# Performance work log

Measured on AMD Instinct MI355X. Metric: run time of the kernel, lower is better.

The kernel has to match this reference:

```python
import jax, jax.numpy as jnp
from jax import lax
import numpy as np

HIDDEN = 512
NUM_LAYERS = 2
NUM_KEYS = 128
BATCH = 256
SEQ = 512


def setup_inputs() -> dict:
    key = jax.random.key(0)
    ks = jax.random.split(key, 16)
    s = 0.05  # keep gates out of saturation
    inp = {
        "x": jax.random.normal(ks[0], (BATCH, SEQ, NUM_KEYS), dtype=jnp.float32),
        # layer 0 (input size NUM_KEYS); PyTorch gate order i,f,g,o stacked on dim0
        "W_ih0": jax.random.normal(ks[1], (4 * HIDDEN, NUM_KEYS), dtype=jnp.float32) * s,
        "W_hh0": jax.random.normal(ks[2], (4 * HIDDEN, HIDDEN), dtype=jnp.float32) * s,
        "b_ih0": jax.random.normal(ks[3], (4 * HIDDEN,), dtype=jnp.float32) * s,
        "b_hh0": jax.random.normal(ks[4], (4 * HIDDEN,), dtype=jnp.float32) * s,
        # layer 1 (input size HIDDEN)
        "W_ih1": jax.random.normal(ks[5], (4 * HIDDEN, HIDDEN), dtype=jnp.float32) * s,
        "W_hh1": jax.random.normal(ks[6], (4 * HIDDEN, HIDDEN), dtype=jnp.float32) * s,
        "b_ih1": jax.random.normal(ks[7], (4 * HIDDEN,), dtype=jnp.float32) * s,
        "b_hh1": jax.random.normal(ks[8], (4 * HIDDEN,), dtype=jnp.float32) * s,
        # final linear head
        "W_fc": jax.random.normal(ks[9], (NUM_KEYS, HIDDEN), dtype=jnp.float32) * s,
        "b_fc": jax.random.normal(ks[10], (NUM_KEYS,), dtype=jnp.float32) * s,
    }
    return inp


def _lstm_layer(xs, W_ih, W_hh, b_ih, b_hh):
    # xs: [B, T, in]. Precompute input contribution to all gates outside the scan.
    B = xs.shape[0]
    H = W_hh.shape[1]
    xg = jnp.einsum("bti,gi->btg", xs, W_ih) + b_ih + b_hh  # [B, T, 4H]

    def step(carry, xg_t):
        h, c = carry
        g = xg_t + h @ W_hh.T  # [B, 4H]
        i, f, gg, o = jnp.split(g, 4, axis=-1)
        i = jax.nn.sigmoid(i)
        f = jax.nn.sigmoid(f)
        gg = jnp.tanh(gg)
        o = jax.nn.sigmoid(o)
        c = f * c + i * gg
        h = o * jnp.tanh(c)
        return (h, c), h

    h0 = jnp.zeros((B, H), xs.dtype)
    (_, _), hs = lax.scan(step, (h0, h0), jnp.swapaxes(xg, 0, 1))  # hs: [T, B, H]
    return jnp.swapaxes(hs, 0, 1)  # [B, T, H]


def reference(x, W_ih0, W_hh0, b_ih0, b_hh0, W_ih1, W_hh1, b_ih1, b_hh1, W_fc, b_fc):
    h = _lstm_layer(x, W_ih0, W_hh0, b_ih0, b_hh0)
    h = _lstm_layer(h, W_ih1, W_hh1, b_ih1, b_hh1)
    return h[:, -1, :] @ W_fc.T + b_fc  # [B, NUM_KEYS]
```

## Files before the change

### kernel.cpp

```cpp
#include <hip/hip_runtime.h>

#define HIDDEN 512
#define TSEQ 512
#define NKEYS 128

typedef short short8_t __attribute__((ext_vector_type(8)));
typedef short short4_t __attribute__((ext_vector_type(4)));
typedef float f32x4 __attribute__((ext_vector_type(4)));
typedef int i32x4 __attribute__((ext_vector_type(4)));

__device__ __forceinline__ ushort f2bf(float f) {
    union { float f; unsigned u; } v; v.f = f;
    unsigned r = (v.u + 0x7FFFu + ((v.u >> 16) & 1u)) >> 16;
    return (ushort)r;
}
__device__ __forceinline__ float sigm(float x) { return 1.0f / (1.0f + __expf(-x)); }
__device__ __forceinline__ float tanh_f(float x) { return 2.0f / (1.0f + __expf(-2.0f * x)) - 1.0f; }

__global__ void cast_w(const float* __restrict__ Wih, const float* __restrict__ Whh,
                       ushort* __restrict__ Wc, int KIN, int K) {
    long idx = (long)blockIdx.x * blockDim.x + threadIdx.x;
    if (idx >= (long)2048 * K) return;
    int row = (int)(idx / K), k = (int)(idx % K);
    float v = (k < KIN) ? Wih[(long)row * KIN + k] : Whh[(long)row * HIDDEN + (k - KIN)];
    Wc[idx] = f2bf(v);
}

__global__ void prep_bias(const float* __restrict__ a, const float* __restrict__ b,
                          const float* __restrict__ c, const float* __restrict__ d,
                          float* __restrict__ b0, float* __restrict__ b1) {
    int i = blockIdx.x * blockDim.x + threadIdx.x;
    if (i < 2048) { b0[i] = a[i] + b[i]; b1[i] = c[i] + d[i]; }
}

__global__ void init_zeros(ushort* __restrict__ h0s, ushort* __restrict__ h1p) {
    int idx = blockIdx.x * blockDim.x + threadIdx.x;
    ushort4 z = {0, 0, 0, 0};
    if (idx < 32768) *(ushort4*)(h0s + (size_t)idx * 4) = z;
    else             *(ushort4*)(h1p + (size_t)(idx - 32768) * 4) = z;
}

#define AF_LIST_20(M) M(0)M(1)M(2)M(3)M(4)M(5)M(6)M(7)M(8)M(9)M(10)M(11)M(12)M(13)M(14)M(15)M(16)M(17)M(18)M(19)
#define AF_LIST_32(M) AF_LIST_20(M) M(20)M(21)M(22)M(23)M(24)M(25)M(26)M(27)M(28)M(29)M(30)M(31)

#define AF_DECL(i) short8_t af##i;
#define AF_LOAD(i) af##i = *(const short8_t*)(wsrc + (i) * 32); \
                   asm volatile("" : "+a"(af##i));

#define AF_MFMA(i) { \
    const char* _b  = ((i) < KSI) ? (bpi + (i) * 64) : (bpr + ((i) - KSI) * 64); \
    const int   _r16 = ((i) < KSI) ? (16 * INROW) : (16 * RECROW); \
    short8_t bf0 = *(const short8_t*)_b; \
    short8_t bf1 = *(const short8_t*)(_b + _r16); \
    if ((i) & 1) { \
        asm("v_mfma_f32_16x16x32_bf16 %0, %1, %2, %0" : "+v"(accA1) : "a"(af##i), "v"(bf0)); \
        asm("v_mfma_f32_16x16x32_bf16 %0, %1, %2, %0" : "+v"(accB1) : "a"(af##i), "v"(bf1)); \
    } else { \
        asm("v_mfma_f32_16x16x32_bf16 %0, %1, %2, %0" : "+v"(accA0) : "a"(af##i), "v"(bf0)); \
        asm("v_mfma_f32_16x16x32_bf16 %0, %1, %2, %0" : "+v"(accB0) : "a"(af##i), "v"(bf1)); \
    } }

template <int L>
__device__ __forceinline__ void lstm_body(
    char* smem, int bid,
    const float* __restrict__ x, const ushort* __restrict__ Wc,
    const float* __restrict__ biasc, ushort* __restrict__ h0s,
    ushort* __restrict__ h1p, float* __restrict__ hlast, int* flags)
{
    constexpr int KIN   = L ? 512 : 128;
    constexpr int K     = KIN + 512;
    constexpr int KSI   = KIN / 32;
    constexpr int INROW = L ? 1056 : 288;
    constexpr int RECROW = 1056;
    constexpr int RECPAR = 32 * RECROW;
    constexpr size_t TSTR = 128 * 1024;

    char* const recb = smem;
    char* const inb  = smem + 2 * RECPAR;

    const int tid = threadIdx.x;
    const int tile = bid & 7;
    const int g    = (bid >> 3) & 15;
    const int b0   = tile * 32;
    const int w = tid >> 6, lane = tid & 63, hi4 = lane >> 4, arow = lane & 15;
    const int Uw = g * 32 + w * 4;
    const int row_l = 512 * (arow & 3) + Uw + (arow >> 2);

    int* const ownbase  = flags + (L ? 4096 : 0) + tile * 512;
    int* const prodbase = flags + tile * 512;
    int* const myflag   = ownbase + g * 32;

    AF_LIST_32(AF_DECL)
    {
        const ushort* wsrc = Wc + (size_t)row_l * K + hi4 * 8;
        if constexpr (L == 0) { AF_LIST_20(AF_LOAD) }
        else                  { AF_LIST_32(AF_LOAD) }
    }
    f32x4 bias4;
#pragma unroll
    for (int r = 0; r < 4; ++r) bias4[r] = biasc[512 * r + Uw + hi4];

    for (int i = tid; i < 2 * RECPAR / 4; i += 512) ((int*)recb)[i] = 0;

    float c0 = 0.0f, c1 = 0.0f;

    const int si = tid >> 4, sj = tid & 15;
    float4 xa, xb;
    if constexpr (L == 0) {
        const float* xp = x + ((size_t)(b0 + si) * TSEQ) * NKEYS + sj * 8;
        xa = *(const float4*)xp; xb = *(const float4*)(xp + 4);
    }

    const int pub = lane >> 2, q = lane & 3;
    const bool notown = pub != g;
    const unsigned long long rflagA = (unsigned long long)(ownbase + pub * 32);
    const unsigned long long iflagA = (unsigned long long)(prodbase + pub * 32);

    __syncthreads();

#pragma unroll 1
    for (int t = 0; t < TSEQ; ++t) {
        const int par = t & 1;
        char* const rb_cur = recb + par * RECPAR;
        char* const rb_nxt = recb + (par ^ 1) * RECPAR;

        if constexpr (L == 0) {
            short8_t s;
            s[0] = (short)f2bf(xa.x); s[1] = (short)f2bf(xa.y);
            s[2] = (short)f2bf(xa.z); s[3] = (short)f2bf(xa.w);
            s[4] = (short)f2bf(xb.x); s[5] = (short)f2bf(xb.y);
            s[6] = (short)f2bf(xb.z); s[7] = (short)f2bf(xb.w);
            *(short8_t*)(inb + si * INROW + sj * 16) = s;
        }

        i32x4 i0, i1, i2, i3, r0, r1, r2, r3;
        {
            int ipend = (L == 1) ? 1 : 0;
            int rpend = notown ? 1 : 0;
            while (true) {
                if (ipend) {
                    int v;
                    asm volatile("global_load_dword %0, %1, off sc0 sc1\n\t"
                                 "s_waitcnt vmcnt(0)"
                                 : "=&v"(v) : "v"(iflagA) : "memory");
                    if (v >= t + 1) {
                        const ushort* ib = h0s + ((size_t)(t + 1)) * TSTR
                                           + ((size_t)tile * 16 + pub) * 1024
                                           + (size_t)w * 128 + q * 8;
                        asm volatile("global_load_dwordx4 %0, %4, off\n\t"
                                     "global_load_dwordx4 %1, %5, off\n\t"
                                     "global_load_dwordx4 %2, %6, off\n\t"
                                     "global_load_dwordx4 %3, %7, off"
                                     : "=&v"(i0), "=&v"(i1), "=&v"(i2), "=&v"(i3)
                                     : "v"((unsigned long long)ib),
                                       "v"((unsigned long long)(ib + 32)),
                                       "v"((unsigned long long)(ib + 64)),
                                       "v"((unsigned long long)(ib + 96))
                                     : "memory");
                        ipend = 0;
                    }
                }
                if (rpend) {
                    int v;
                    asm volatile("global_load_dword %0, %1, off sc0 sc1\n\t"
                                 "s_waitcnt vmcnt(0)"
                                 : "=&v"(v) : "v"(rflagA) : "memory");
                    if (v >= t) {
                        if constexpr (L == 0) {
                            const ushort* rb = h0s + ((size_t)t) * TSTR
                                               + ((size_t)tile * 16 + pub) * 1024
                                               + (size_t)w * 128 + q * 8;
                            asm volatile("global_load_dwordx4 %0, %4, off\n\t"
                                         "global_load_dwordx4 %1, %5, off\n\t"
                                         "global_load_dwordx4 %2, %6, off\n\t"
                                         "global_load_dwordx4 %3, %7, off"
                                         : "=&v"(r0), "=&v"(r1), "=&v"(r2), "=&v"(r3)
                                         : "v"((unsigned long long)rb),
                                           "v"((unsigned long long)(rb + 32)),
                                           "v"((unsigned long long)(rb + 64)),
                                           "v"((unsigned long long)(rb + 96))
                                         : "memory");
                        } else {
                            const ushort* rb = h1p + (((size_t)par * 8 + tile) * 16 + pub) * 1024
                                               + (size_t)w * 128 + q * 8;
                            asm volatile("global_load_dwordx4 %0, %4, off sc0 sc1\n\t"
                                         "global_load_dwordx4 %1, %5, off sc0 sc1\n\t"
                                         "global_load_dwordx4 %2, %6, off sc0 sc1\n\t"
                                         "global_load_dwordx4 %3, %7, off sc0 sc1"
                                         : "=&v"(r0), "=&v"(r1), "=&v"(r2), "=&v"(r3)
                                         : "v"((unsigned long long)rb),
                                           "v"((unsigned long long)(rb + 32)),
                                           "v"((unsigned long long)(rb + 64)),
                                           "v"((unsigned long long)(rb + 96))
                                         : "memory");
                        }
                        rpend = 0;
                    }
                }
                if (__all((ipend | rpend) == 0)) break;
                __builtin_amdgcn_s_sleep(1);
            }
            asm volatile("s_waitcnt vmcnt(0)" ::: "memory");
            if constexpr (L == 1) {
                *(i32x4*)(inb + (w * 4 + 0) * INROW + pub * 64 + q * 16) = i0;
                *(i32x4*)(inb + (w * 4 + 1) * INROW + pub * 64 + q * 16) = i1;
                *(i32x4*)(inb + (w * 4 + 2) * INROW + pub * 64 + q * 16) = i2;
                *(i32x4*)(inb + (w * 4 + 3) * INROW + pub * 64 + q * 16) = i3;
            }
            if (notown) {
                *(i32x4*)(rb_cur + (w * 4 + 0) * RECROW + pub * 64 + q * 16) = r0;
                *(i32x4*)(rb_cur + (w * 4 + 1) * RECROW + pub * 64 + q * 16) = r1;
                *(i32x4*)(rb_cur + (w * 4 + 2) * RECROW + pub * 64 + q * 16) = r2;
                *(i32x4*)(rb_cur + (w * 4 + 3) * RECROW + pub * 64 + q * 16) = r3;
            }
        }
        if constexpr (L == 0) {
            const int tt = (t + 1) & 511;
            const float* xp = x + ((size_t)(b0 + si) * TSEQ + tt) * NKEYS + sj * 8;
            xa = *(const float4*)xp; xb = *(const float4*)(xp + 4);
        }
        __syncthreads();

        f32x4 accA0 = bias4, accB0 = bias4;
        f32x4 accA1 = {0.f, 0.f, 0.f, 0.f}, accB1 = {0.f, 0.f, 0.f, 0.f};
        const char* bpi = inb + arow * INROW + hi4 * 16;
        const char* bpr = rb_cur + arow * RECROW + hi4 * 16;
        if constexpr (L == 0) { AF_LIST_20(AF_MFMA) }
        else                  { AF_LIST_32(AF_MFMA) }
        asm volatile("s_nop 7\n\ts_nop 7"
                     : "+v"(accA0), "+v"(accA1), "+v"(accB0), "+v"(accB1));
        f32x4 am0 = accA0 + accA1, am1 = accB0 + accB1;

        float ig0 = sigm(am0[0]), fg0 = sigm(am0[1]);
        float gg0 = tanh_f(am0[2]), og0 = sigm(am0[3]);
        c0 = fg0 * c0 + ig0 * gg0;
        float h0f = og0 * tanh_f(c0);
        float ig1 = sigm(am1[0]), fg1 = sigm(am1[1]);
        float gg1 = tanh_f(am1[2]), og1 = sigm(am1[3]);
        c1 = fg1 * c1 + ig1 * gg1;
        float h1f = og1 * tanh_f(c1);
        int hv0 = f2bf(h0f), hv1 = f2bf(h1f);

        *(ushort*)(rb_nxt + arow * RECROW + (Uw + hi4) * 2)        = (ushort)hv0;
        *(ushort*)(rb_nxt + (16 + arow) * RECROW + (Uw + hi4) * 2) = (ushort)hv1;

        int a0 = __shfl(hv0, arow, 64),      a1 = __shfl(hv0, 16 + arow, 64);
        int a2 = __shfl(hv0, 32 + arow, 64), a3 = __shfl(hv0, 48 + arow, 64);
        int e0 = __shfl(hv1, arow, 64),      e1 = __shfl(hv1, 16 + arow, 64);
        int e2 = __shfl(hv1, 32 + arow, 64), e3 = __shfl(hv1, 48 + arow, 64);
        if (hi4 == 0) {
            unsigned lo0 = (a0 & 0xFFFF) | (a1 << 16);
            unsigned hi0 = (a2 & 0xFFFF) | (a3 << 16);
            unsigned long long pk0 = lo0 | ((unsigned long long)hi0 << 32);
            unsigned lo1 = (e0 & 0xFFFF) | (e1 << 16);
            unsigned hi1 = (e2 & 0xFFFF) | (e3 << 16);
            unsigned long long pk1 = lo1 | ((unsigned long long)hi1 << 32);
            ushort* chunk;
            if constexpr (L == 0)
                chunk = h0s + ((size_t)(t + 1)) * TSTR + ((size_t)tile * 16 + g) * 1024;
            else
                chunk = h1p + (((size_t)((t + 1) & 1) * 8 + tile) * 16 + g) * 1024;
            asm volatile("global_store_dwordx2 %0, %2, off sc0 sc1\n\t"
                         "global_store_dwordx2 %1, %3, off sc0 sc1"
                         :: "v"((unsigned long long)(chunk + arow * 32 + w * 4)),
                            "v"((unsigned long long)(chunk + (16 + arow) * 32 + w * 4)),
                            "v"(pk0), "v"(pk1) : "memory");
        }
        if (L == 1 && t == TSEQ - 1) {
            hlast[(size_t)(b0 + arow) * 512 + Uw + hi4]      = h0f;
            hlast[(size_t)(b0 + 16 + arow) * 512 + Uw + hi4] = h1f;
        }

        asm volatile("s_waitcnt vmcnt(0)" ::: "memory");
        __syncthreads();
        if (tid == 0)
            asm volatile("global_store_dword %0, %1, off sc0 sc1"
                         :: "v"((unsigned long long)myflag), "v"(t + 1) : "memory");
    }
}

__global__ __attribute__((amdgpu_waves_per_eu(2, 2))) __launch_bounds__(512)
void lstm_fused(const float* __restrict__ x,
                const ushort* __restrict__ Wc0, const ushort* __restrict__ Wc1,
                const float* __restrict__ bg0, const float* __restrict__ bg1,
                ushort* __restrict__ h0s, ushort* __restrict__ h1p,
                float* __restrict__ hlast, int* flags)
{
    __shared__ __align__(16) char smem[101376];
    const int bid = blockIdx.x;
    if (bid < 128) lstm_body<0>(smem, bid, x, Wc0, bg0, h0s, h1p, hlast, flags);
    else           lstm_body<1>(smem, bid, x, Wc1, bg1, h0s, h1p, hlast, flags);
}

__global__ void fc_kernel(const float* __restrict__ hlast, const float* __restrict__ Wfc,
                          const float* __restrict__ bfc, float* __restrict__ out) {
    __shared__ float hs[HIDDEN];
    const int b = blockIdx.x, n = threadIdx.x;
    for (int k = n; k < HIDDEN; k += 128) hs[k] = hlast[b * HIDDEN + k];
    __syncthreads();
    const float* wr = Wfc + (long)n * HIDDEN;
    float acc = bfc[n];
#pragma unroll 8
    for (int k = 0; k < HIDDEN; ++k) acc += hs[k] * wr[k];
    out[b * 128 + n] = acc;
}

extern "C" void kernel_launch(void* const* d_in, const int* in_sizes, int n_in,
                              void* d_out, int out_size, void* d_ws, size_t ws_size,
                              hipStream_t stream) {
    const float* x    = (const float*)d_in[0];
    const float* Wih0 = (const float*)d_in[1];
    const float* Whh0 = (const float*)d_in[2];
    const float* bih0 = (const float*)d_in[3];
    const float* bhh0 = (const float*)d_in[4];
    const float* Wih1 = (const float*)d_in[5];
    const float* Whh1 = (const float*)d_in[6];
    const float* bih1 = (const float*)d_in[7];
    const float* bhh1 = (const float*)d_in[8];
    const float* Wfc  = (const float*)d_in[9];
    const float* bfc  = (const float*)d_in[10];

    char* ws = (char*)d_ws;
    size_t off = 0;
    auto alloc = [&](size_t bytes) {
        void* p = ws + off;
        off = (off + bytes + 255) & ~(size_t)255;
        return p;
    };
    ushort* Wc0   = (ushort*)alloc(2048UL * 640 * 2);
    ushort* Wc1   = (ushort*)alloc(2048UL * 1024 * 2);
    float*  bg0   = (float*)alloc(2048 * 4);
    float*  bg1   = (float*)alloc(2048 * 4);
    float*  hlast = (float*)alloc(256UL * 512 * 4);
    ushort* h1p   = (ushort*)alloc(2UL * 128 * 1024 * 2);
    int*    flags = (int*)alloc(65536);
    ushort* h0s   = (ushort*)alloc(513UL * 128 * 1024 * 2);
    if (ws_size < off) return;

    hipMemsetAsync(flags, 0, 65536, stream);
    init_zeros<<<256, 256, 0, stream>>>(h0s, h1p);
    cast_w<<<(2048 * 640  + 255) / 256, 256, 0, stream>>>(Wih0, Whh0, Wc0, 128, 640);
    cast_w<<<(2048 * 1024 + 255) / 256, 256, 0, stream>>>(Wih1, Whh1, Wc1, 512, 1024);
    prep_bias<<<8, 256, 0, stream>>>(bih0, bhh0, bih1, bhh1, bg0, bg1);

    {
        void* args[] = { (void*)&x, (void*)&Wc0, (void*)&Wc1, (void*)&bg0, (void*)&bg1,
                         (void*)&h0s, (void*)&h1p, (void*)&hlast, (void*)&flags };
        hipLaunchCooperativeKernel((const void*)lstm_fused, dim3(256), dim3(512),
                                   args, 0, stream);
    }

    fc_kernel<<<256, 128, 0, stream>>>(hlast, Wfc, bfc, (float*)d_out);
}
```

Before: 1.973 ms.

## Use per-wave progress flags and double-buffered input smem to drop block barrier

Each wave now publishes its own progress flag after storing its slice of h, instead of the whole block syncing and thread 0 publishing one flag. Consumers poll the per-wave flags of the waves that produce the data they gather. The exchange layout of h in global memory is transposed so each wave writes a contiguous chunk, and the gather scatters that data into shared memory with 8-byte writes. The input staging buffer is double-buffered by timestep parity so the end-of-step __syncthreads can be removed, at the cost of more LDS, a larger flag array and more flag polling traffic.

```diff
diff --git a/kernel.cpp b/kernel.cpp
--- a/kernel.cpp
+++ b/kernel.cpp
@@ -8,6 +8,7 @@
 typedef short short4_t __attribute__((ext_vector_type(4)));
 typedef float f32x4 __attribute__((ext_vector_type(4)));
 typedef int i32x4 __attribute__((ext_vector_type(4)));
+typedef int i32x2 __attribute__((ext_vector_type(2)));
 
 __device__ __forceinline__ ushort f2bf(float f) {
     union { float f; unsigned u; } v; v.f = f;
@@ -59,6 +60,11 @@
         asm("v_mfma_f32_16x16x32_bf16 %0, %1, %2, %0" : "+v"(accA0) : "a"(af##i), "v"(bf0)); \
         asm("v_mfma_f32_16x16x32_bf16 %0, %1, %2, %0" : "+v"(accB0) : "a"(af##i), "v"(bf1)); \
     } }
+
+#define SCAT2(base, stride, uo, r0_, REG) { \
+    i32x2 _lo, _hi; _lo[0] = REG[0]; _lo[1] = REG[1]; _hi[0] = REG[2]; _hi[1] = REG[3]; \
+    *(i32x2*)((base) + (r0_) * (stride) + (uo)) = _lo; \
+    *(i32x2*)((base) + ((r0_) + 1) * (stride) + (uo)) = _hi; }
 
 template <int L>
 __device__ __forceinline__ void lstm_body(
@@ -73,6 +79,7 @@
     constexpr int INROW = L ? 1056 : 288;
     constexpr int RECROW = 1056;
     constexpr int RECPAR = 32 * RECROW;
+    constexpr int INPAR  = 32 * INROW;
     constexpr size_t TSTR = 128 * 1024;
 
     char* const recb = smem;
@@ -86,9 +93,15 @@
     const int Uw = g * 32 + w * 4;
     const int row_l = 512 * (arow & 3) + Uw + (arow >> 2);
 
-    int* const ownbase  = flags + (L ? 4096 : 0) + tile * 512;
-    int* const prodbase = flags + tile * 512;
-    int* const myflag   = ownbase + g * 32;
+    const int cpub = tid >> 5, cwv = (tid >> 2) & 7, cqt = tid & 3;
+    const int uoff = (cpub * 32 + cwv * 4) * 2;
+    const bool notown = (cpub != g);
+
+    int* const flagL = flags + (L ? 32768 : 0) + tile * 4096;
+    int* const flagP = flags + tile * 4096;
+    const unsigned long long rflagA = (unsigned long long)(flagL + (cpub * 8 + cwv) * 32);
+    const unsigned long long iflagA = (unsigned long long)(flagP + (cpub * 8 + cwv) * 32);
+    const unsigned long long myflagA = (unsigned long long)(flagL + (g * 8 + w) * 32);
 
     AF_LIST_32(AF_DECL)
     {
@@ -111,11 +124,6 @@
         xa = *(const float4*)xp; xb = *(const float4*)(xp + 4);
     }
 
-    const int pub = lane >> 2, q = lane & 3;
-    const bool notown = pub != g;
-    const unsigned long long rflagA = (unsigned long long)(ownbase + pub * 32);
-    const unsigned long long iflagA = (unsigned long long)(prodbase + pub * 32);
-
     __syncthreads();
 
 #pragma unroll 1
@@ -123,6 +131,7 @@
         const int par = t & 1;
         char* const rb_cur = recb + par * RECPAR;
         char* const rb_nxt = recb + (par ^ 1) * RECPAR;
+        char* const in_cur = inb + par * INPAR;
 
         if constexpr (L == 0) {
             short8_t s;
@@ -130,10 +139,10 @@
             s[2] = (short)f2bf(xa.z); s[3] = (short)f2bf(xa.w);
             s[4] = (short)f2bf(xb.x); s[5] = (short)f2bf(xb.y);
             s[6] = (short)f2bf(xb.z); s[7] = (short)f2bf(xb.w);
-            *(short8_t*)(inb + si * INROW + sj * 16) = s;
-        }
-
-        i32x4 i0, i1, i2, i3, r0, r1, r2, r3;
+            *(short8_t*)(in_cur + si * INROW + sj * 16) = s;
+        }
+
+        i32x4 ia0, ia1, ia2, ia3, rr0, rr1, rr2, rr3;
         {
             int ipend = (L == 1) ? 1 : 0;
             int rpend = notown ? 1 : 0;
@@ -144,18 +153,18 @@
                                  "s_waitcnt vmcnt(0)"
                                  : "=&v"(v) : "v"(iflagA) : "memory");
                     if (v >= t + 1) {
-                        const ushort* ib = h0s + ((size_t)(t + 1)) * TSTR
-                                           + ((size_t)tile * 16 + pub) * 1024
-                                           + (size_t)w * 128 + q * 8;
+                        const ushort* p = h0s + ((size_t)(t + 1)) * TSTR
+                                          + ((size_t)tile * 16 + cpub) * 1024
+                                          + cwv * 128 + cqt * 32;
                         asm volatile("global_load_dwordx4 %0, %4, off\n\t"
                                      "global_load_dwordx4 %1, %5, off\n\t"
                                      "global_load_dwordx4 %2, %6, off\n\t"
                                      "global_load_dwordx4 %3, %7, off"
-                                     : "=&v"(i0), "=&v"(i1), "=&v"(i2), "=&v"(i3)
-                                     : "v"((unsigned long long)ib),
-                                       "v"((unsigned long long)(ib + 32)),
-                                       "v"((unsigned long long)(ib + 64)),
-                                       "v"((unsigned long long)(ib + 96))
+                                     : "=&v"(ia0), "=&v"(ia1), "=&v"(ia2), "=&v"(ia3)
+                                     : "v"((unsigned long long)p),
+                                       "v"((unsigned long long)(p + 8)),
+                                       "v"((unsigned long long)(p + 16)),
+                                       "v"((unsigned long long)(p + 24))
                                      : "memory");
                         ipend = 0;
                     }
@@ -167,31 +176,31 @@
                                  : "=&v"(v) : "v"(rflagA) : "memory");
                     if (v >= t) {
                         if constexpr (L == 0) {
-                            const ushort* rb = h0s + ((size_t)t) * TSTR
-                                               + ((size_t)tile * 16 + pub) * 1024
-                                               + (size_t)w * 128 + q * 8;
+                            const ushort* p = h0s + ((size_t)t) * TSTR
+                                              + ((size_t)tile * 16 + cpub) * 1024
+                                              + cwv * 128 + cqt * 32;
                             asm volatile("global_load_dwordx4 %0, %4, off\n\t"
                                          "global_load_dwordx4 %1, %5, off\n\t"
                                          "global_load_dwordx4 %2, %6, off\n\t"
                                          "global_load_dwordx4 %3, %7, off"
-                                         : "=&v"(r0), "=&v"(r1), "=&v"(r2), "=&v"(r3)
-                                         : "v"((unsigned long long)rb),
-                                           "v"((unsigned long long)(rb + 32)),
-                                           "v"((unsigned long long)(rb + 64)),
-                                           "v"((unsigned long long)(rb + 96))
+                                         : "=&v"(rr0), "=&v"(rr1), "=&v"(rr2), "=&v"(rr3)
+                                         : "v"((unsigned long long)p),
+                                           "v"((unsigned long long)(p + 8)),
+                                           "v"((unsigned long long)(p + 16)),
+                                           "v"((unsigned long long)(p + 24))
                                          : "memory");
                         } else {
-                            const ushort* rb = h1p + (((size_t)par * 8 + tile) * 16 + pub) * 1024
-                                               + (size_t)w * 128 + q * 8;
+                            const ushort* p = h1p + (((size_t)par * 8 + tile) * 16 + cpub) * 1024
+                                              + cwv * 128 + cqt * 32;
                             asm volatile("global_load_dwordx4 %0, %4, off sc0 sc1\n\t"
                                          "global_load_dwordx4 %1, %5, off sc0 sc1\n\t"
                                          "global_load_dwordx4 %2, %6, off sc0 sc1\n\t"
                                          "global_load_dwordx4 %3, %7, off sc0 sc1"
-                                         : "=&v"(r0), "=&v"(r1), "=&v"(r2), "=&v"(r3)
-                                         : "v"((unsigned long long)rb),
-                                           "v"((unsigned long long)(rb + 32)),
-                                           "v"((unsigned long long)(rb + 64)),
-                                           "v"((unsigned long long)(rb + 96))
+                                         : "=&v"(rr0), "=&v"(rr1), "=&v"(rr2), "=&v"(rr3)
+                                         : "v"((unsigned long long)p),
+                                           "v"((unsigned long long)(p + 8)),
+                                           "v"((unsigned long long)(p + 16)),
+                                           "v"((unsigned long long)(p + 24))
                                          : "memory");
                         }
                         rpend = 0;
@@ -201,17 +210,18 @@
                 __builtin_amdgcn_s_sleep(1);
             }
             asm volatile("s_waitcnt vmcnt(0)" ::: "memory");
+            const int r0_ = cqt * 8;
             if constexpr (L == 1) {
-                *(i32x4*)(inb + (w * 4 + 0) * INROW + pub * 64 + q * 16) = i0;
-                *(i32x4*)(inb + (w * 4 + 1) * INROW + pub * 64 + q * 16) = i1;
-                *(i32x4*)(inb + (w * 4 + 2) * INROW + pub * 64 + q * 16) = i2;
-                *(i32x4*)(inb + (w * 4 + 3) * INROW + pub * 64 + q * 16) = i3;
+                SCAT2(in_cur, INROW, uoff, r0_ + 0, ia0)
+                SCAT2(in_cur, INROW, uoff, r0_ + 2, ia1)
+                SCAT2(in_cur, INROW, uoff, r0_ + 4, ia2)
+                SCAT2(in_cur, INROW, uoff, r0_ + 6, ia3)
             }
             if (notown) {
-                *(i32x4*)(rb_cur + (w * 4 + 0) * RECROW + pub * 64 + q * 16) = r0;
-                *(i32x4*)(rb_cur + (w * 4 + 1) * RECROW + pub * 64 + q * 16) = r1;
-                *(i32x4*)(rb_cur + (w * 4 + 2) * RECROW + pub * 64 + q * 16) = r2;
-                *(i32x4*)(rb_cur + (w * 4 + 3) * RECROW + pub * 64 + q * 16) = r3;
+                SCAT2(rb_cur, RECROW, uoff, r0_ + 0, rr0)
+                SCAT2(rb_cur, RECROW, uoff, r0_ + 2, rr1)
+                SCAT2(rb_cur, RECROW, uoff, r0_ + 4, rr2)
+                SCAT2(rb_cur, RECROW, uoff, r0_ + 6, rr3)
             }
         }
         if constexpr (L == 0) {
@@ -223,7 +233,7 @@
 
         f32x4 accA0 = bias4, accB0 = bias4;
         f32x4 accA1 = {0.f, 0.f, 0.f, 0.f}, accB1 = {0.f, 0.f, 0.f, 0.f};
-        const char* bpi = inb + arow * INROW + hi4 * 16;
+        const char* bpi = in_cur + arow * INROW + hi4 * 16;
         const char* bpr = rb_cur + arow * RECROW + hi4 * 16;
         if constexpr (L == 0) { AF_LIST_20(AF_MFMA) }
         else                  { AF_LIST_32(AF_MFMA) }
@@ -262,8 +272,8 @@
                 chunk = h1p + (((size_t)((t + 1) & 1) * 8 + tile) * 16 + g) * 1024;
             asm volatile("global_store_dwordx2 %0, %2, off sc0 sc1\n\t"
                          "global_store_dwordx2 %1, %3, off sc0 sc1"
-                         :: "v"((unsigned long long)(chunk + arow * 32 + w * 4)),
-                            "v"((unsigned long long)(chunk + (16 + arow) * 32 + w * 4)),
+                         :: "v"((unsigned long long)(chunk + w * 128 + arow * 4)),
+                            "v"((unsigned long long)(chunk + w * 128 + (16 + arow) * 4)),
                             "v"(pk0), "v"(pk1) : "memory");
         }
         if (L == 1 && t == TSEQ - 1) {
@@ -272,10 +282,9 @@
         }
 
         asm volatile("s_waitcnt vmcnt(0)" ::: "memory");
-        __syncthreads();
-        if (tid == 0)
+        if (lane == 0)
             asm volatile("global_store_dword %0, %1, off sc0 sc1"
-                         :: "v"((unsigned long long)myflag), "v"(t + 1) : "memory");
+                         :: "v"(myflagA), "v"(t + 1) : "memory");
     }
 }
 
@@ -286,7 +295,7 @@
                 ushort* __restrict__ h0s, ushort* __restrict__ h1p,
                 float* __restrict__ hlast, int* flags)
 {
-    __shared__ __align__(16) char smem[101376];
+    __shared__ __align__(16) char smem[135168];
     const int bid = blockIdx.x;
     if (bid < 128) lstm_body<0>(smem, bid, x, Wc0, bg0, h0s, h1p, hlast, flags);
     else           lstm_body<1>(smem, bid, x, Wc1, bg1, h0s, h1p, hlast, flags);
@@ -333,11 +342,11 @@
     float*  bg1   = (float*)alloc(2048 * 4);
     float*  hlast = (float*)alloc(256UL * 512 * 4);
     ushort* h1p   = (ushort*)alloc(2UL * 128 * 1024 * 2);
-    int*    flags = (int*)alloc(65536);
+    int*    flags = (int*)alloc(262144);
     ushort* h0s   = (ushort*)alloc(513UL * 128 * 1024 * 2);
     if (ws_size < off) return;
 
-    hipMemsetAsync(flags, 0, 65536, stream);
+    hipMemsetAsync(flags, 0, 262144, stream);
     init_zeros<<<256, 256, 0, stream>>>(h0s, h1p);
     cast_w<<<(2048 * 640  + 255) / 256, 256, 0, stream>>>(Wih0, Whh0, Wc0, 128, 640);
     cast_w<<<(2048 * 1024 + 255) / 256, 256, 0, stream>>>(Wih1, Whh1, Wc1, 512, 1024);
```

New measurement: 2.543 ms. 28.9% more time.

## Poll cross-block flags from one wave and broadcast readiness via LDS

Applied to the files above, without the earlier changes.

Only wave 0 of each block now spins on the global producer flags with system-scope loads. It publishes the observed flag values into a small LDS array that the other waves spin on before issuing their data loads. The aim is to cut global polling traffic and cache-coherence pressure, since 8 waves each polling the same flags becomes 1. In exchange there is an extra LDS handoff hop on the critical path of every timestep. It also relies on the volatile LDS ordering plus the following waitcnt/barrier to keep the data loads correctly ordered after the flag observation.

```diff
diff --git a/kernel.cpp b/kernel.cpp
--- a/kernel.cpp
+++ b/kernel.cpp
@@ -77,6 +77,8 @@
 
     char* const recb = smem;
     char* const inb  = smem + 2 * RECPAR;
+    volatile int* const arrR = (volatile int*)(smem + 101376);
+    volatile int* const arrI = arrR + 16;
 
     const int tid = threadIdx.x;
     const int tile = bid & 7;
@@ -101,6 +103,7 @@
     for (int r = 0; r < 4; ++r) bias4[r] = biasc[512 * r + Uw + hi4];
 
     for (int i = tid; i < 2 * RECPAR / 4; i += 512) ((int*)recb)[i] = 0;
+    if (tid < 32) arrR[tid] = 0;
 
     float c0 = 0.0f, c1 = 0.0f;
 
@@ -137,68 +140,120 @@
         {
             int ipend = (L == 1) ? 1 : 0;
             int rpend = notown ? 1 : 0;
-            while (true) {
+            if (w == 0) {
+                while (true) {
+                    if (ipend) {
+                        int v;
+                        asm volatile("global_load_dword %0, %1, off sc0 sc1\n\t"
+                                     "s_waitcnt vmcnt(0)"
+                                     : "=&v"(v) : "v"(iflagA) : "memory");
+                        if (v >= t + 1) {
+                            arrI[pub] = v;
+                            const ushort* p = h0s + ((size_t)(t + 1)) * TSTR
+                                              + ((size_t)tile * 16 + pub) * 1024
+                                              + (size_t)w * 128 + q * 8;
+                            asm volatile("global_load_dwordx4 %0, %4, off\n\t"
+                                         "global_load_dwordx4 %1, %5, off\n\t"
+                                         "global_load_dwordx4 %2, %6, off\n\t"
+                                         "global_load_dwordx4 %3, %7, off"
+                                         : "=&v"(i0), "=&v"(i1), "=&v"(i2), "=&v"(i3)
+                                         : "v"((unsigned long long)p),
+                                           "v"((unsigned long long)(p + 32)),
+                                           "v"((unsigned long long)(p + 64)),
+                                           "v"((unsigned long long)(p + 96))
+                                         : "memory");
+                            ipend = 0;
+                        }
+                    }
+                    if (rpend) {
+                        int v;
+                        asm volatile("global_load_dword %0, %1, off sc0 sc1\n\t"
+                                     "s_waitcnt vmcnt(0)"
+                                     : "=&v"(v) : "v"(rflagA) : "memory");
+                        if (v >= t) {
+                            arrR[pub] = v;
+                            if constexpr (L == 0) {
+                                const ushort* p = h0s + ((size_t)t) * TSTR
+                                                  + ((size_t)tile * 16 + pub) * 1024
+                                                  + (size_t)w * 128 + q * 8;
+                                asm volatile("global_load_dwordx4 %0, %4, off\n\t"
+                                             "global_load_dwordx4 %1, %5, off\n\t"
+                                             "global_load_dwordx4 %2, %6, off\n\t"
+                                             "global_load_dwordx4 %3, %7, off"
+                                             : "=&v"(r0), "=&v"(r1), "=&v"(r2), "=&v"(r3)
+                                             : "v"((unsigned long long)p),
+                                               "v"((unsigned long long)(p + 32)),
+                                               "v"((unsigned long long)(p + 64)),
+                                               "v"((unsigned long long)(p + 96))
+                                             : "memory");
+                            } else {
+                                const ushort* p = h1p + (((size_t)par * 8 + tile) * 16 + pub) * 1024
+                                                  + (size_t)w * 128 + q * 8;
+                                asm volatile("global_load_dwordx4 %0, %4, off sc0 sc1\n\t"
+                                             "global_load_dwordx4 %1, %5, off sc0 sc1\n\t"
+                                             "global_load_dwordx4 %2, %6, off sc0 sc1\n\t"
+                                             "global_load_dwordx4 %3, %7, off sc0 sc1"
+                                             : "=&v"(r0), "=&v"(r1), "=&v"(r2), "=&v"(r3)
+                                             : "v"((unsigned long long)p),
+                                               "v"((unsigned long long)(p + 32)),
+                                               "v"((unsigned long long)(p + 64)),
+                                               "v"((unsigned long long)(p + 96))
+                                             : "memory");
+                            }
+                            rpend = 0;
+                        }
+                    }
+                    if (__all((ipend | rpend) == 0)) break;
+                    __builtin_amdgcn_s_sleep(1);
+                }
+            } else {
                 if (ipend) {
-                    int v;
-                    asm volatile("global_load_dword %0, %1, off sc0 sc1\n\t"
-                                 "s_waitcnt vmcnt(0)"
-                                 : "=&v"(v) : "v"(iflagA) : "memory");
-                    if (v >= t + 1) {
-                        const ushort* ib = h0s + ((size_t)(t + 1)) * TSTR
-                                           + ((size_t)tile * 16 + pub) * 1024
-                                           + (size_t)w * 128 + q * 8;
+                    while (arrI[pub] < t + 1) __builtin_amdgcn_s_sleep(0);
+                    const ushort* p = h0s + ((size_t)(t + 1)) * TSTR
+                                      + ((size_t)tile * 16 + pub) * 1024
+                                      + (size_t)w * 128 + q * 8;
+                    asm volatile("global_load_dwordx4 %0, %4, off\n\t"
+                                 "global_load_dwordx4 %1, %5, off\n\t"
+                                 "global_load_dwordx4 %2, %6, off\n\t"
+                                 "global_load_dwordx4 %3, %7, off"
+                                 : "=&v"(i0), "=&v"(i1), "=&v"(i2), "=&v"(i3)
+                                 : "v"((unsigned long long)p),
+                                   "v"((unsigned long long)(p + 32)),
+                                   "v"((unsigned long long)(p + 64)),
+                                   "v"((unsigned long long)(p + 96))
+                                 : "memory");
+                }
+                if (rpend) {
+                    while (arrR[pub] < t) __builtin_amdgcn_s_sleep(0);
+                    if constexpr (L == 0) {
+                        const ushort* p = h0s + ((size_t)t) * TSTR
+                                          + ((size_t)tile * 16 + pub) * 1024
+                                          + (size_t)w * 128 + q * 8;
                         asm volatile("global_load_dwordx4 %0, %4, off\n\t"
                                      "global_load_dwordx4 %1, %5, off\n\t"
                                      "global_load_dwordx4 %2, %6, off\n\t"
                                      "global_load_dwordx4 %3, %7, off"
-                                     : "=&v"(i0), "=&v"(i1), "=&v"(i2), "=&v"(i3)
-                                     : "v"((unsigned long long)ib),
-                                       "v"((unsigned long long)(ib + 32)),
-                                       "v"((unsigned long long)(ib + 64)),
-                                       "v"((unsigned long long)(ib + 96))
+                                     : "=&v"(r0), "=&v"(r1), "=&v"(r2), "=&v"(r3)
+                                     : "v"((unsigned long long)p),
+                                       "v"((unsigned long long)(p + 32)),
+                                       "v"((unsigned long long)(p + 64)),
+                                       "v"((unsigned long long)(p + 96))
                                      : "memory");
-                        ipend = 0;
+                    } else {
+                        const ushort* p = h1p + (((size_t)par * 8 + tile) * 16 + pub) * 1024
+                                          + (size_t)w * 128 + q * 8;
+                        asm volatile("global_load_dwordx4 %0, %4, off sc0 sc1\n\t"
+                                     "global_load_dwordx4 %1, %5, off sc0 sc1\n\t"
+                                     "global_load_dwordx4 %2, %6, off sc0 sc1\n\t"
+                                     "global_load_dwordx4 %3, %7, off sc0 sc1"
+                                     : "=&v"(r0), "=&v"(r1), "=&v"(r2), "=&v"(r3)
+                                     : "v"((unsigned long long)p),
+                                       "v"((unsigned long long)(p + 32)),
+                                       "v"((unsigned long long)(p + 64)),
+                                       "v"((unsigned long long)(p + 96))
+                                     : "memory");
                     }
                 }
-                if (rpend) {
-                    int v;
-                    asm volatile("global_load_dword %0, %1, off sc0 sc1\n\t"
-                                 "s_waitcnt vmcnt(0)"
-                                 : "=&v"(v) : "v"(rflagA) : "memory");
-                    if (v >= t) {
-                        if constexpr (L == 0) {
-                            const ushort* rb = h0s + ((size_t)t) * TSTR
-                                               + ((size_t)tile * 16 + pub) * 1024
-                                               + (size_t)w * 128 + q * 8;
-                            asm volatile("global_load_dwordx4 %0, %4, off\n\t"
-                                         "global_load_dwordx4 %1, %5, off\n\t"
-                                         "global_load_dwordx4 %2, %6, off\n\t"
-                                         "global_load_dwordx4 %3, %7, off"
-                                         : "=&v"(r0), "=&v"(r1), "=&v"(r2), "=&v"(r3)
-                                         : "v"((unsigned long long)rb),
-                                           "v"((unsigned long long)(rb + 32)),
-                                           "v"((unsigned long long)(rb + 64)),
-                                           "v"((unsigned long long)(rb + 96))
-                                         : "memory");
-                        } else {
-                            const ushort* rb = h1p + (((size_t)par * 8 + tile) * 16 + pub) * 1024
-                                               + (size_t)w * 128 + q * 8;
-                            asm volatile("global_load_dwordx4 %0, %4, off sc0 sc1\n\t"
-                                         "global_load_dwordx4 %1, %5, off sc0 sc1\n\t"
-                                         "global_load_dwordx4 %2, %6, off sc0 sc1\n\t"
-                                         "global_load_dwordx4 %3, %7, off sc0 sc1"
-                                         : "=&v"(r0), "=&v"(r1), "=&v"(r2), "=&v"(r3)
-                                         : "v"((unsigned long long)rb),
-                                           "v"((unsigned long long)(rb + 32)),
-                                           "v"((unsigned long long)(rb + 64)),
-                                           "v"((unsigned long long)(rb + 96))
-                                         : "memory");
-                        }
-                        rpend = 0;
-                    }
-                }
-                if (__all((ipend | rpend) == 0)) break;
-                __builtin_amdgcn_s_sleep(1);
             }
             asm volatile("s_waitcnt vmcnt(0)" ::: "memory");
             if constexpr (L == 1) {
@@ -286,7 +341,7 @@
                 ushort* __restrict__ h0s, ushort* __restrict__ h1p,
                 float* __restrict__ hlast, int* flags)
 {
-    __shared__ __align__(16) char smem[101376];
+    __shared__ __align__(16) char smem[101504];
     const int bid = blockIdx.x;
     if (bid < 128) lstm_body<0>(smem, bid, x, Wc0, bg0, h0s, h1p, hlast, flags);
     else           lstm_body<1>(smem, bid, x, Wc1, bg1, h0s, h1p, hlast, flags);
```

Result: faster. 1.859 ms (-5.8%).
